# Optimization experiments

Measured on AMD Instinct MI355X. Metric: run time of the kernel, lower is better.

## Reference

```python
import jax, jax.numpy as jnp
import numpy as np

DEPTH = 4  # truncation depth of the signature


def setup_inputs() -> dict:
    key = jax.random.key(0)
    # path: (batch, stream, channels)
    path = jax.random.normal(key, (128, 128, 12), dtype=jnp.float32)
    return {"path": path}


def _exp_terms(d, depth):
    """Tensor exponential of a single linear increment d: (B, C).

    Returns a tuple of flattened levels; level k has shape (B, C**k) and
    equals d^{\otimes k} / k!.
    """
    B = d.shape[0]
    terms = [d]
    for k in range(2, depth + 1):
        terms.append(jnp.einsum('bi,bj->bij', terms[-1], d).reshape(B, -1) / k)
    return tuple(terms)


def _signature(path, depth):
    """Truncated path signature (stream=False, basepoint=False).

    Combines per-increment tensor exponentials with Chen's identity:
    (A \otimes B)_m = A_m + B_m + sum_{i=1}^{m-1} A_i \otimes B_{m-i}.
    """
    B, L, C = path.shape
    dx = path[:, 1:] - path[:, :-1]  # (B, L-1, C) path increments
    init = _exp_terms(dx[:, 0], depth)

    def step(sig, d):
        e = _exp_terms(d, depth)
        new = []
        for m in range(1, depth + 1):  # signature level m, shape (B, C**m)
            t = sig[m - 1] + e[m - 1]
            for i in range(1, m):  # cross terms sig_i (x) e_{m-i}
                t = t + jnp.einsum('bi,bj->bij', sig[i - 1], e[m - i - 1]).reshape(B, -1)
            new.append(t)
        return tuple(new), None

    # scan over the remaining L-2 increments (time-major)
    sig, _ = jax.lax.scan(step, init, jnp.transpose(dx[:, 1:], (1, 0, 2)))
    # flatten levels in order 1..depth, matching signatory's layout
    return jnp.concatenate(sig, axis=-1)  # (B, C + C^2 + ... + C^depth)


def reference(path):
    return _signature(path, DEPTH)
```

## Files before the change

### kernel.cpp

```cpp
#include <hip/hip_runtime.h>


#define NC    12
#define NPTS  128
#define NSTEP 128
#define OUT_PER_B 22620
#define B1 384
#define B2 448
#define PADQ 33

typedef float vf16 __attribute__((ext_vector_type(16)));
typedef const vf16 __attribute__((address_space(4))) c4_vf16;

#define WGET(e) ((e) < 16 ? w0[(e) & 15] : ((e) < 32 ? w1[(e) & 15] : w2[(e) & 15]))

__global__ __launch_bounds__(B1)
void prep_kernel(const float* __restrict__ path, float* __restrict__ Draw,
                 float* __restrict__ DTg) {
    const int b = blockIdx.x;
    const int t = threadIdx.x;
    const int c  = t >> 5;
    const int sq = t & 31;
    const float* pb = path + (size_t)b * (NPTS * NC);
    float d[4];
    #pragma unroll
    for (int e = 0; e < 4; ++e) {
        int s = 4 * sq + e;
        d[e] = (s < NPTS - 1) ? (pb[(s + 1) * NC + c] - pb[s * NC + c]) : 0.f;
        Draw[(size_t)b * 1536 + s * NC + c] = d[e];
    }
    float4* dtg = (float4*)(DTg + (size_t)b * 1536 + c * NSTEP);
    dtg[sq] = make_float4(d[0], d[1], d[2], d[3]);
}

__global__ __launch_bounds__(B2, 4)
void sig_kernel(const float* __restrict__ Draw, const float* __restrict__ DTg,
                float* __restrict__ out) {
    const int bid = blockIdx.x;
    const int b  = bid >> 2;
    const int iq = bid & 3;
    const int t  = threadIdx.x;

    __shared__ __align__(16) float4 DT4[NC * PADQ];

    if (t < NC * 32) {
        int c = t >> 5, sq = t & 31;
        const float4* src = (const float4*)(DTg + (size_t)b * 1536 + c * NSTEP);
        DT4[c * PADQ + sq] = src[sq];
    }
    __syncthreads();

    const int ta  = (t < 432) ? t : (t - 432);
    const int il  = ta / 144;
    const int rem = ta - il * 144;
    const int j   = rem / 12;
    const int k   = rem - j * 12;
    const int i   = iq * 3 + il;

    float acc[12];
    #pragma unroll
    for (int l = 0; l < 12; ++l) acc[l] = 0.f;
    float s3 = 0.f, s2 = 0.f, s1 = 0.f;

    unsigned long long base_u;
    {
        unsigned long long a = (unsigned long long)(Draw + (size_t)b * 1536);
        unsigned int lo = __builtin_amdgcn_readfirstlane((unsigned int)a);
        unsigned int hi = __builtin_amdgcn_readfirstlane((unsigned int)(a >> 32));
        base_u = ((unsigned long long)hi << 32) | lo;
    }
    const c4_vf16* wp = (const c4_vf16*)base_u;

    const float4* dti = &DT4[i * PADQ];
    const float4* dtj = &DT4[j * PADQ];
    const float4* dtk = &DT4[k * PADQ];

    for (int sq = 0; sq < NSTEP / 4; ++sq) {
        vf16 w0 = wp[3 * sq + 0];
        vf16 w1 = wp[3 * sq + 1];
        vf16 w2 = wp[3 * sq + 2];

        float4 di4 = dti[sq];
        float4 dj4 = dtj[sq];
        float4 dk4 = dtk[sq];

        #pragma unroll
        for (int u = 0; u < 4; ++u) {
            const float di = (&di4.x)[u];
            const float dj = (&dj4.x)[u];
            const float dk = (&dk4.x)[u];

            float A4 = (s1 + 0.25f * di) * (1.f / 3.f);
            float B4 = (s2 + dj * A4) * 0.5f;
            float C3 = s3 + dk * B4;

            #pragma unroll
            for (int l = 0; l < 12; ++l)
                acc[l] += C3 * WGET(12 * u + l);

            float A3 = (s1 + di * (1.f / 3.f)) * 0.5f;
            float C2 = s2 + dj * A3;
            s3 += dk * C2;
            s2 += dj * (s1 + 0.5f * di);
            s1 += di;
        }
    }

    if (t < 432) {
        float* ob = out + (size_t)b * OUT_PER_B;
        if (j == 0 && k == 0) ob[i] = s1;
        if (k == 0) ob[12 + i * 12 + j] = s2;
        const int ijk = (i * 12 + j) * 12 + k;
        ob[156 + ijk] = s3;
        float4* o4 = (float4*)(ob + 1884 + (size_t)ijk * 12);
        o4[0] = make_float4(acc[0], acc[1], acc[2],  acc[3]);
        o4[1] = make_float4(acc[4], acc[5], acc[6],  acc[7]);
        o4[2] = make_float4(acc[8], acc[9], acc[10], acc[11]);
    }
}

extern "C" void kernel_launch(void* const* d_in, const int* in_sizes, int n_in,
                              void* d_out, int out_size, void* d_ws, size_t ws_size,
                              hipStream_t stream) {
    const float* path = (const float*)d_in[0];
    float* out = (float*)d_out;
    const int nbatch = in_sizes[0] / (NPTS * NC);

    float* Draw = (float*)d_ws;
    float* DTg  = Draw + (size_t)nbatch * 1536;

    prep_kernel<<<nbatch, B1, 0, stream>>>(path, Draw, DTg);
    sig_kernel<<<nbatch * 4, B2, 0, stream>>>(Draw, DTg, out);
}
```

Measured before the change: 82.50 us.

## Fuse increment prep into signature kernel and broadcast level-4 weights via readlane

Removes the separate prep kernel. Each block now loads the raw path into shared memory and computes its own increments. The scalar-load vector fetch of the 12 increments per step is replaced by a per-lane LDS read plus 12 readlane broadcasts. Work is also re-split across the 4 blocks per batch so that each block takes a j/k half-quadrant instead of a slice of i. This saves a launch and a global round-trip, but every block redundantly computes the increments and the readlane calls add VALU/SALU work in the inner loop.

```diff
diff --git a/kernel.cpp b/kernel.cpp
--- a/kernel.cpp
+++ b/kernel.cpp
@@ -3,92 +3,74 @@
 
 #define NC    12
 #define NPTS  128
-#define NSTEP 128
 #define OUT_PER_B 22620
-#define B1 384
-#define B2 448
-#define PADQ 33
+#define BLOCK 448
+#define PADQ  33
 
-typedef float vf16 __attribute__((ext_vector_type(16)));
-typedef const vf16 __attribute__((address_space(4))) c4_vf16;
-
-#define WGET(e) ((e) < 16 ? w0[(e) & 15] : ((e) < 32 ? w1[(e) & 15] : w2[(e) & 15]))
-
-__global__ __launch_bounds__(B1)
-void prep_kernel(const float* __restrict__ path, float* __restrict__ Draw,
-                 float* __restrict__ DTg) {
-    const int b = blockIdx.x;
-    const int t = threadIdx.x;
-    const int c  = t >> 5;
-    const int sq = t & 31;
-    const float* pb = path + (size_t)b * (NPTS * NC);
-    float d[4];
-    #pragma unroll
-    for (int e = 0; e < 4; ++e) {
-        int s = 4 * sq + e;
-        d[e] = (s < NPTS - 1) ? (pb[(s + 1) * NC + c] - pb[s * NC + c]) : 0.f;
-        Draw[(size_t)b * 1536 + s * NC + c] = d[e];
-    }
-    float4* dtg = (float4*)(DTg + (size_t)b * 1536 + c * NSTEP);
-    dtg[sq] = make_float4(d[0], d[1], d[2], d[3]);
+__device__ __forceinline__ float rl(float v, int lane) {
+    return __int_as_float(__builtin_amdgcn_readlane(__float_as_int(v), lane));
 }
 
-__global__ __launch_bounds__(B2, 4)
-void sig_kernel(const float* __restrict__ Draw, const float* __restrict__ DTg,
-                float* __restrict__ out) {
+__global__ __launch_bounds__(BLOCK, 4)
+void sig_kernel(const float* __restrict__ path, float* __restrict__ out) {
     const int bid = blockIdx.x;
     const int b  = bid >> 2;
-    const int iq = bid & 3;
+    const int q  = bid & 3;
+    const int jq = q >> 1;
+    const int kq = q & 1;
     const int t  = threadIdx.x;
 
     __shared__ __align__(16) float4 DT4[NC * PADQ];
+    __shared__ __align__(16) float4 P4[NPTS * NC / 4];
 
-    if (t < NC * 32) {
-        int c = t >> 5, sq = t & 31;
-        const float4* src = (const float4*)(DTg + (size_t)b * 1536 + c * NSTEP);
-        DT4[c * PADQ + sq] = src[sq];
+    const float4* pb4 = (const float4*)(path + (size_t)b * (NPTS * NC));
+    if (t < 384) P4[t] = pb4[t];
+    __syncthreads();
+    if (t < 384) {
+        const int c  = t >> 5;
+        const int sq = t & 31;
+        const float* P = (const float*)P4;
+        float d[4];
+        #pragma unroll
+        for (int e = 0; e < 4; ++e) {
+            int s = 4 * sq + e;
+            d[e] = (s < NPTS - 1) ? (P[(s + 1) * NC + c] - P[s * NC + c]) : 0.f;
+        }
+        DT4[c * PADQ + sq] = make_float4(d[0], d[1], d[2], d[3]);
     }
     __syncthreads();
 
     const int ta  = (t < 432) ? t : (t - 432);
-    const int il  = ta / 144;
-    const int rem = ta - il * 144;
-    const int j   = rem / 12;
-    const int k   = rem - j * 12;
-    const int i   = iq * 3 + il;
+    const int i   = ta / 36;
+    const int r   = ta - i * 36;
+    const int jl  = r / 6;
+    const int kl  = r - jl * 6;
+    const int j   = jq * 6 + jl;
+    const int k   = kq * 6 + kl;
 
     float acc[12];
     #pragma unroll
     for (int l = 0; l < 12; ++l) acc[l] = 0.f;
     float s3 = 0.f, s2 = 0.f, s1 = 0.f;
 
-    unsigned long long base_u;
-    {
-        unsigned long long a = (unsigned long long)(Draw + (size_t)b * 1536);
-        unsigned int lo = __builtin_amdgcn_readfirstlane((unsigned int)a);
-        unsigned int hi = __builtin_amdgcn_readfirstlane((unsigned int)(a >> 32));
-        base_u = ((unsigned long long)hi << 32) | lo;
-    }
-    const c4_vf16* wp = (const c4_vf16*)base_u;
-
+    const int lane = t & 63;
     const float4* dti = &DT4[i * PADQ];
     const float4* dtj = &DT4[j * PADQ];
     const float4* dtk = &DT4[k * PADQ];
+    const float4* dtv = &DT4[(lane < 12 ? lane : 11) * PADQ];
 
-    for (int sq = 0; sq < NSTEP / 4; ++sq) {
-        vf16 w0 = wp[3 * sq + 0];
-        vf16 w1 = wp[3 * sq + 1];
-        vf16 w2 = wp[3 * sq + 2];
-
+    for (int sq = 0; sq < 32; ++sq) {
         float4 di4 = dti[sq];
         float4 dj4 = dtj[sq];
         float4 dk4 = dtk[sq];
+        float4 dv4 = dtv[sq];
 
         #pragma unroll
         for (int u = 0; u < 4; ++u) {
             const float di = (&di4.x)[u];
             const float dj = (&dj4.x)[u];
             const float dk = (&dk4.x)[u];
+            const float dv = (&dv4.x)[u];
 
             float A4 = (s1 + 0.25f * di) * (1.f / 3.f);
             float B4 = (s2 + dj * A4) * 0.5f;
@@ -96,7 +78,7 @@
 
             #pragma unroll
             for (int l = 0; l < 12; ++l)
-                acc[l] += C3 * WGET(12 * u + l);
+                acc[l] += C3 * rl(dv, l);
 
             float A3 = (s1 + di * (1.f / 3.f)) * 0.5f;
             float C2 = s2 + dj * A3;
@@ -108,8 +90,8 @@
 
     if (t < 432) {
         float* ob = out + (size_t)b * OUT_PER_B;
-        if (j == 0 && k == 0) ob[i] = s1;
-        if (k == 0) ob[12 + i * 12 + j] = s2;
+        if (q == 0 && jl == 0 && kl == 0) ob[i] = s1;
+        if (kl == 0) ob[12 + i * 12 + j] = s2;
         const int ijk = (i * 12 + j) * 12 + k;
         ob[156 + ijk] = s3;
         float4* o4 = (float4*)(ob + 1884 + (size_t)ijk * 12);
@@ -125,10 +107,5 @@
     const float* path = (const float*)d_in[0];
     float* out = (float*)d_out;
     const int nbatch = in_sizes[0] / (NPTS * NC);
-
-    float* Draw = (float*)d_ws;
-    float* DTg  = Draw + (size_t)nbatch * 1536;
-
-    prep_kernel<<<nbatch, B1, 0, stream>>>(path, Draw, DTg);
-    sig_kernel<<<nbatch * 4, B2, 0, stream>>>(Draw, DTg, out);
+    sig_kernel<<<nbatch * 4, BLOCK, 0, stream>>>(path, out);
 }
```

After: 89.81 us. 1.09x slower.
